# Kernel tuning notes

Hardware: AMD Instinct MI355X
Metric: run time of the kernel (lower is better)

The kernel has to match this reference:

```python
import jax, jax.numpy as jnp
import numpy as np

N = 16384          # nodes
E = 262144         # edges (before self-loops)
FIN_N, FIN_E = 768, 64
F, FE = 256, 128   # node/edge channels
H, C = 8, 32       # heads, per-head dim (H*C == F)
L = 2              # num GATv2 modules
NEG_SLOPE = 0.2


def layer_norm(x, g, b, eps=1e-5):
    mu = jnp.mean(x, axis=-1, keepdims=True)
    var = jnp.mean((x - mu) ** 2, axis=-1, keepdims=True)
    return (x - mu) * jax.lax.rsqrt(var + eps) * g + b


def segment_softmax(logits, seg, n):
    # logits: [Et, H], seg: [Et] destination node ids
    m = jax.ops.segment_max(logits, seg, num_segments=n)
    m = jnp.where(jnp.isfinite(m), m, 0.0)
    e = jnp.exp(logits - m[seg])
    s = jax.ops.segment_sum(e, seg, num_segments=n)
    return e / (s[seg] + 1e-16)


def setup_inputs() -> dict:
    key = jax.random.key(0)
    ks = jax.random.split(key, 20)
    inp = {
        "node_feats": jax.random.normal(ks[0], (N, FIN_N), jnp.float32),
        "edge_index": jax.random.randint(ks[1], (2, E), 0, N, dtype=jnp.int32),
        "edge_attr": jax.random.normal(ks[2], (E, FIN_E), jnp.float32),
        # input projections (bias=False)
        "init_node_w": jax.random.normal(ks[3], (F, FIN_N), jnp.float32) * 0.02,
        "init_edge_w": jax.random.normal(ks[4], (FE, FIN_E), jnp.float32) * 0.02,
        # per-layer GATv2 params, stacked on leading layer dim L
        "lin_l_w": jax.random.normal(ks[5], (L, H * C, F), jnp.float32) * 0.05,
        "lin_l_b": jnp.zeros((L, H * C), jnp.float32),
        "lin_r_w": jax.random.normal(ks[6], (L, H * C, F), jnp.float32) * 0.05,
        "lin_r_b": jnp.zeros((L, H * C), jnp.float32),
        "lin_edge_w": jax.random.normal(ks[7], (L, H * C, FE), jnp.float32) * 0.05,
        "att": jax.random.normal(ks[8], (L, H, C), jnp.float32) * 0.05,
        "gat_bias": jnp.zeros((L, H * C), jnp.float32),
        # block params
        "ln1_g": jnp.ones((L, F), jnp.float32), "ln1_b": jnp.zeros((L, F), jnp.float32),
        "mlp_w1": jax.random.normal(ks[9], (L, 2 * F, F), jnp.float32) * 0.05,
        "mlp_w2": jax.random.normal(ks[10], (L, F, 2 * F), jnp.float32) * 0.05,
        "ln2_g": jnp.ones((L, F), jnp.float32), "ln2_b": jnp.zeros((L, F), jnp.float32),
    }
    return inp


def _gatv2_module(x, src, dst, e_emb, p, l, n):
    # e_emb: [Et, H, C] already projected edge embeddings (incl. self-loops)
    x_l = (x @ p["lin_l_w"][l].T + p["lin_l_b"][l]).reshape(n, H, C)
    x_r = (x @ p["lin_r_w"][l].T + p["lin_r_b"][l]).reshape(n, H, C)
    m = x_l[src] + x_r[dst] + e_emb                    # [Et, H, C]
    g = jnp.where(m >= 0, m, NEG_SLOPE * m)            # leaky_relu(0.2)
    logits = jnp.einsum('ehc,hc->eh', g, p["att"][l])
    alpha = segment_softmax(logits, dst, n)            # [Et, H]
    out = jax.ops.segment_sum(alpha[:, :, None] * x_l[src], dst, num_segments=n)
    out = out.reshape(n, H * C) + p["gat_bias"][l]
    # residual -> LN -> MLP -> residual -> LN  (dropout=0, eval mode)
    h = layer_norm(x + out, p["ln1_g"][l], p["ln1_b"][l])
    y = jax.nn.gelu(h @ p["mlp_w1"][l].T, approximate=False) @ p["mlp_w2"][l].T
    return layer_norm(h + y, p["ln2_g"][l], p["ln2_b"][l])


def reference(node_feats, edge_index, edge_attr, init_node_w, init_edge_w,
              lin_l_w, lin_l_b, lin_r_w, lin_r_b, lin_edge_w, att, gat_bias,
              ln1_g, ln1_b, mlp_w1, mlp_w2, ln2_g, ln2_b):
    p = dict(lin_l_w=lin_l_w, lin_l_b=lin_l_b, lin_r_w=lin_r_w, lin_r_b=lin_r_b,
             lin_edge_w=lin_edge_w, att=att, gat_bias=gat_bias, ln1_g=ln1_g,
             ln1_b=ln1_b, mlp_w1=mlp_w1, mlp_w2=mlp_w2, ln2_g=ln2_g, ln2_b=ln2_b)
    x = node_feats @ init_node_w.T                     # [N, F]
    ea = edge_attr @ init_edge_w.T                     # [E, FE]
    src, dst = edge_index[0], edge_index[1]
    # add self loops with fill_value='mean' (mean of incoming edge_attr per node)
    cnt = jax.ops.segment_sum(jnp.ones((E,), ea.dtype), dst, num_segments=N)
    loop_attr = jax.ops.segment_sum(ea, dst, num_segments=N) / jnp.maximum(cnt, 1.0)[:, None]
    ea_all = jnp.concatenate([ea, loop_attr], axis=0)  # [E+N, FE]
    ar = jnp.arange(N, dtype=src.dtype)
    src_all = jnp.concatenate([src, ar])
    dst_all = jnp.concatenate([dst, ar])
    for l in range(L):
        e_emb = (ea_all @ lin_edge_w[l].T).reshape(-1, H, C)
        x = _gatv2_module(x, src_all, dst_all, e_emb, p, l, N)
    return x
```

## Files before the change

kernel.cpp:

```cpp
#include <hip/hip_runtime.h>

typedef unsigned short u16;
typedef __attribute__((ext_vector_type(8))) short s8v;
typedef __attribute__((ext_vector_type(4))) float f4v;

#define NN 16384
#define EE 262144
#define ET (EE + NN)
#define NTILES (ET / 64)

__device__ __forceinline__ float bfu(u16 h){ return __uint_as_float((unsigned)h << 16); }
__device__ __forceinline__ u16 f2bf(float f){
  unsigned u = __float_as_uint(f);
  unsigned r = u + 0x7FFFu + ((u >> 16) & 1u);
  return (u16)(r >> 16);
}
__device__ __forceinline__ float ldf(const void* p, size_t i, int isbf){
  return isbf ? bfu(((const u16*)p)[i]) : ((const float*)p)[i];
}
__device__ __forceinline__ float gelu_f(float x){ return 0.5f*x*(1.0f+erff(x*0.7071067811865475f)); }

__device__ __forceinline__ uint4 load8bf(const void* p, size_t eoff, int isbf){
  if (isbf) return *(const uint4*)((const u16*)p + eoff);
  const float* f = (const float*)p + eoff;
  uint4 r;
  r.x = (unsigned)f2bf(f[0]) | ((unsigned)f2bf(f[1])<<16);
  r.y = (unsigned)f2bf(f[2]) | ((unsigned)f2bf(f[3])<<16);
  r.z = (unsigned)f2bf(f[4]) | ((unsigned)f2bf(f[5])<<16);
  r.w = (unsigned)f2bf(f[6]) | ((unsigned)f2bf(f[7])<<16);
  return r;
}

__device__ __forceinline__ void gload16(const void* g, void* l){
  __builtin_amdgcn_global_load_lds((const __attribute__((address_space(1))) void*)g,
                                   (__attribute__((address_space(3))) void*)l, 16, 0, 0);
}

__global__ void k_detect(const void* nf, int* flag)
{
  int t = threadIdx.x;
  const float* f = (const float*)nf;
  int cnt = 0;
  for (int i = t; i < 4096; i += 256) {
    float a = fabsf(f[i]);
    if (a > 1e-5f && a < 100.0f) cnt++;
  }
  __shared__ int s[256];
  s[t] = cnt; __syncthreads();
  for (int st = 128; st > 0; st >>= 1) { if (t < st) s[t] += s[t+st]; __syncthreads(); }
  if (t == 0) *flag = (s[0] < 2048) ? 1 : 0;
}

__global__ void k_cvt(const void* __restrict__ in, u16* __restrict__ out, const int* __restrict__ dflag)
{
  int isbf = *dflag;
  size_t i = ((size_t)blockIdx.x*256 + threadIdx.x)*8;
  *(uint4*)&out[i] = load8bf(in, i, isbf);
}

__global__ void k_wcvt(const void* __restrict__ lw, const void* __restrict__ rw,
                       const void* __restrict__ w1, const void* __restrict__ w2,
                       const void* __restrict__ iw, u16* __restrict__ wall,
                       const int* __restrict__ dflag)
{
  int isbf = *dflag;
  size_t i = ((size_t)blockIdx.x*256 + threadIdx.x)*8;
  const void* src; size_t off;
  if (i < 196608) { src = iw; off = i; }
  else {
    size_t j = i - 196608;
    size_t l = j / 393216; j -= l*393216;
    if (j < 65536)       { src = lw; off = l*65536 + j; }
    else if (j < 131072) { src = rw; off = l*65536 + (j - 65536); }
    else if (j < 262144) { src = w1; off = l*131072 + (j - 131072); }
    else                 { src = w2; off = l*131072 + (j - 262144); }
  }
  *(uint4*)&wall[i] = load8bf(src, off, isbf);
}

template<int KK, int NJ, int ACT, int CFMT>
__global__ __launch_bounds__(256)
void mg3(const u16* __restrict__ A, const u16* __restrict__ B,
         const void* __restrict__ bias1, const void* __restrict__ bias2,
         size_t bioff, int nsplit, int has_bias,
         void* __restrict__ C, void* __restrict__ C2, int N,
         const int* __restrict__ dflag)
{
  constexpr int NIT = KK/32;
  constexpr int NBF = 4*NJ;
  __shared__ u16 As[2][4][512];
  __shared__ u16 Bs[2][NBF][512];
  int isbf = *dflag;
  int t = threadIdx.x;
  int w = t>>6, lane = t&63, l4 = lane&15, quad = lane>>4;
  int bm = blockIdx.y*64, bn = blockIdx.x*(64*NJ);

  const u16* gA = A + (size_t)(bm + w*16 + l4)*KK + quad*8;
  const u16* gB[NJ];
  #pragma unroll
  for (int j=0;j<NJ;++j)
    gB[j] = B + (size_t)(bn + (NJ*w + j)*16 + l4)*KK + quad*8;

  f4v acc[4][NJ];
  f4v zero = {0.f,0.f,0.f,0.f};
  #pragma unroll
  for (int i=0;i<4;++i)
    #pragma unroll
    for (int j=0;j<NJ;++j) acc[i][j] = zero;

  gload16(gA, &As[0][w][0]);
  #pragma unroll
  for (int j=0;j<NJ;++j) gload16(gB[j], &Bs[0][NJ*w + j][0]);
  __syncthreads();

  int buf = 0;
  for (int it = 0; it < NIT; ++it) {
    if (it + 1 < NIT) {
      int k0 = (it+1)*32;
      gload16(gA + k0, &As[buf^1][w][0]);
      #pragma unroll
      for (int j=0;j<NJ;++j) gload16(gB[j] + k0, &Bs[buf^1][NJ*w + j][0]);
    }
    s8v a[4], b[NJ];
    #pragma unroll
    for (int i=0;i<4;++i) a[i] = *(const s8v*)&As[buf][i][lane*8];
    #pragma unroll
    for (int j=0;j<NJ;++j) b[j] = *(const s8v*)&Bs[buf][NJ*w + j][lane*8];
    #pragma unroll
    for (int i=0;i<4;++i)
      #pragma unroll
      for (int j=0;j<NJ;++j)
        acc[i][j] = __builtin_amdgcn_mfma_f32_16x16x32_bf16(a[i], b[j], acc[i][j], 0,0,0);
    __syncthreads();
    buf ^= 1;
  }

  #pragma unroll
  for (int i=0;i<4;++i)
    #pragma unroll
    for (int j=0;j<NJ;++j) {
      int cj = bn + (NJ*w + j)*16 + l4;
      float bvs = 0.f;
      if (has_bias) bvs = (cj < nsplit) ? ldf(bias1, bioff + cj, isbf)
                                        : ldf(bias2, bioff + cj - nsplit, isbf);
      #pragma unroll
      for (int r=0;r<4;++r) {
        int row = bm + i*16 + quad*4 + r;
        float v = acc[i][j][r] + bvs;
        if (ACT==1) v = gelu_f(v);
        if (CFMT==1) ((u16*)C)[(size_t)row*N + cj] = f2bf(v);
        else {
          ((float*)C)[(size_t)row*N + cj] = v;
          if (CFMT==2) ((u16*)C2)[(size_t)row*N + cj] = f2bf(v);
        }
      }
    }
}

__global__ void k_count(const int* __restrict__ dst, int* __restrict__ deg)
{
  int e = blockIdx.x*256 + threadIdx.x;
  if (e >= ET) return;
  int d = (e < EE) ? dst[e] : (e - EE);
  atomicAdd(&deg[d], 1);
}

__global__ void k_scan(const int* __restrict__ deg, int* __restrict__ rowstart)
{
  __shared__ int csum[256];
  int t = threadIdx.x;
  int s = 0;
  for (int i=0;i<64;i++) s += deg[t*64+i];
  csum[t] = s;
  __syncthreads();
  if (t == 0) {
    int r = 0;
    for (int i=0;i<256;i++){ int v = csum[i]; csum[i] = r; r += v; }
    rowstart[NN] = r;
  }
  __syncthreads();
  int b = csum[t];
  for (int i=0;i<64;i++){ rowstart[t*64+i] = b; b += deg[t*64+i]; }
}

__global__ void k_scatter(const int* __restrict__ src, const int* __restrict__ dst,
                          const int* __restrict__ rowstart,
                          int* __restrict__ fill, int* __restrict__ csr,
                          int* __restrict__ srcc, int* __restrict__ dstc)
{
  int e = blockIdx.x*256 + threadIdx.x;
  if (e >= ET) return;
  int d  = (e < EE) ? dst[e] : (e - EE);
  int sv = (e < EE) ? src[e] : (e - EE);
  int pos = rowstart[d] + atomicAdd(&fill[d], 1);
  csr[pos]  = e;
  srcc[pos] = sv;
  dstc[pos] = d;
}

__global__ void k_loopmean(const int* __restrict__ csr, const int* __restrict__ rowstart,
                           const void* __restrict__ edge_attr, u16* __restrict__ loopmean,
                           const int* __restrict__ dflag)
{
  int isbf = *dflag;
  int n = blockIdx.x, j = threadIdx.x;
  int s = rowstart[n], e1 = rowstart[n+1];
  float sum = 0.f; int cnt = 0;
  for (int p = s; p < e1; ++p) {
    int eid = csr[p];
    if (eid < EE) { sum += ldf(edge_attr, (size_t)eid*64 + j, isbf); cnt++; }
  }
  loopmean[(size_t)n*64 + j] = f2bf(sum / (float)max(cnt, 1));
}

__global__ void k_wc(const void* __restrict__ We, const void* __restrict__ iew,
                     u16* __restrict__ Wcb, const int* __restrict__ dflag)
{
  int isbf = *dflag;
  int idx = blockIdx.x*256 + threadIdx.x;
  int j = idx & 63, c = (idx >> 6) & 255, l = idx >> 14;
  float s = 0.f;
  for (int k=0;k<128;k++) s += ldf(We, ((size_t)l*256 + c)*128 + k, isbf) * ldf(iew, (size_t)k*64 + j, isbf);
  Wcb[idx] = f2bf(s);
}

__global__ __launch_bounds__(256)
void k_elogits(const int* __restrict__ csr, const int* __restrict__ srcc, const int* __restrict__ dstc,
               const u16* __restrict__ Wcb, const u16* __restrict__ xlr,
               const void* __restrict__ edge_attr, const u16* __restrict__ loopmean,
               const void* __restrict__ att, size_t att_off,
               float* __restrict__ logits, const int* __restrict__ dflag)
{
  int isbf = *dflag;
  __shared__ u16 WcF[32*64*8];
  __shared__ u16 attr_s[64*72];
  __shared__ float satt[256];
  __shared__ int ssrc[64], sdst[64];

  int t = threadIdx.x;
  int w = t>>6, lane = t&63, l4 = lane&15, quad = lane>>4;

  satt[t] = ldf(att, att_off + t, isbf);
  #pragma unroll
  for (int f = 0; f < 8; ++f) {
    int fr = w + f*4;
    int i = fr >> 1, ks = fr & 1;
    *(uint4*)&WcF[(fr*64 + lane)*8] = *(const uint4*)&Wcb[(size_t)(16*i + l4)*64 + ks*32 + quad*8];
  }

  f4v zero = {0.f,0.f,0.f,0.f};
  for (int tile = blockIdx.x; tile < NTILES; tile += gridDim.x) {
    int e0 = tile*64;
    __syncthreads();
    if (t < 64) {
      ssrc[t] = srcc[e0 + t];
      sdst[t] = dstc[e0 + t];
    }
    {
      int er = t >> 2, part = t & 3;
      int eid = csr[e0 + er];
      uint4 v0, v1;
      if (eid < EE) {
        v0 = load8bf(edge_attr, (size_t)eid*64 + part*16,     isbf);
        v1 = load8bf(edge_attr, (size_t)eid*64 + part*16 + 8, isbf);
      } else {
        v0 = *(const uint4*)&loopmean[(size_t)(eid-EE)*64 + part*16];
        v1 = *(const uint4*)&loopmean[(size_t)(eid-EE)*64 + part*16 + 8];
      }
      *(uint4*)&attr_s[er*72 + part*16]     = v0;
      *(uint4*)&attr_s[er*72 + part*16 + 8] = v1;
    }
    __syncthreads();

    s8v b0 = *(const s8v*)&attr_s[(w*16 + l4)*72 + quad*8];
    s8v b1 = *(const s8v*)&attr_s[(w*16 + l4)*72 + 32 + quad*8];
    f4v acc[16];
    #pragma unroll
    for (int i=0;i<16;++i){
      s8v a0 = *(const s8v*)&WcF[((2*i  )*64 + lane)*8];
      s8v a1 = *(const s8v*)&WcF[((2*i+1)*64 + lane)*8];
      acc[i] = __builtin_amdgcn_mfma_f32_16x16x32_bf16(a0, b0, zero, 0,0,0);
      acc[i] = __builtin_amdgcn_mfma_f32_16x16x32_bf16(a1, b1, acc[i], 0,0,0);
    }

    int me = w*16 + l4;
    int sn = ssrc[me], dn = sdst[me];
    float ph[8] = {0.f,0.f,0.f,0.f,0.f,0.f,0.f,0.f};
    #pragma unroll
    for (int i=0;i<16;++i){
      uint2 xlv = *(const uint2*)&xlr[(size_t)sn*512 +       i*16 + quad*4];
      uint2 xrv = *(const uint2*)&xlr[(size_t)dn*512 + 256 + i*16 + quad*4];
      float4 av = *(const float4*)&satt[i*16 + quad*4];
      float m0 = acc[i][0] + bfu((u16)(xlv.x & 0xffff)) + bfu((u16)(xrv.x & 0xffff));
      float m1 = acc[i][1] + bfu((u16)(xlv.x >> 16))    + bfu((u16)(xrv.x >> 16));
      float m2 = acc[i][2] + bfu((u16)(xlv.y & 0xffff)) + bfu((u16)(xrv.y & 0xffff));
      float m3 = acc[i][3] + bfu((u16)(xlv.y >> 16))    + bfu((u16)(xrv.y >> 16));
      float g0 = fmaxf(m0, 0.2f*m0), g1 = fmaxf(m1, 0.2f*m1);
      float g2 = fmaxf(m2, 0.2f*m2), g3 = fmaxf(m3, 0.2f*m3);
      ph[i>>1] += av.x*g0 + av.y*g1 + av.z*g2 + av.w*g3;
    }
    #pragma unroll
    for (int h=0;h<8;++h){
      ph[h] += __shfl_xor(ph[h], 16);
      ph[h] += __shfl_xor(ph[h], 32);
    }
    if (quad == 0){
      float4 lo = {ph[0], ph[1], ph[2], ph[3]};
      float4 hi = {ph[4], ph[5], ph[6], ph[7]};
      *(float4*)&logits[(size_t)(e0 + me)*8]     = lo;
      *(float4*)&logits[(size_t)(e0 + me)*8 + 4] = hi;
    }
  }
}

__global__ __launch_bounds__(256)
void k_aggln(const int* __restrict__ srcc, const int* __restrict__ rowstart,
             const float* __restrict__ logits, const u16* __restrict__ xlr, const float* __restrict__ xbuf,
             const void* __restrict__ gat_bias, const void* __restrict__ ln1g, const void* __restrict__ ln1b,
             size_t poff, float* __restrict__ hbuf, u16* __restrict__ hbufb, const int* __restrict__ dflag)
{
  int isbf = *dflag;
  int lane = threadIdx.x & 63, wid = threadIdx.x >> 6;
  int n = blockIdx.x*4 + wid;
  int s = rowstart[n], deg = rowstart[n+1] - s;
  int myh = lane >> 3;
  float mrun = -3.0e38f, lrun = 0.f;
  float a0=0.f, a1=0.f, a2=0.f, a3=0.f;

  for (int c0 = 0; c0 < deg; c0 += 64) {
    int idx = s + c0 + lane; if (idx >= ET) idx = ET-1;
    int sv = srcc[idx];
    int lim = min(64, deg - c0);
    size_t lbase = (size_t)(s + c0)*8 + myh;
    for (int j = 0; j < lim; ++j) {
      int sn  = __shfl(sv, j);
      float lg = logits[lbase + (size_t)j*8];
      uint2 xv = *(const uint2*)&xlr[(size_t)sn*512 + 4*lane];
      float mn = fmaxf(mrun, lg);
      float sc = __expf(mrun - mn);
      float wv = __expf(lg - mn);
      mrun = mn;
      lrun = lrun*sc + wv;
      a0 = a0*sc + wv*bfu((u16)(xv.x & 0xffff));
      a1 = a1*sc + wv*bfu((u16)(xv.x >> 16));
      a2 = a2*sc + wv*bfu((u16)(xv.y & 0xffff));
      a3 = a3*sc + wv*bfu((u16)(xv.y >> 16));
    }
  }
  float inv = 1.f/(lrun + 1e-16f);
  int c = 4*lane;
  float4 res = *(const float4*)&xbuf[(size_t)n*256 + c];
  float o0 = a0*inv + ldf(gat_bias, poff+c+0, isbf) + res.x;
  float o1 = a1*inv + ldf(gat_bias, poff+c+1, isbf) + res.y;
  float o2 = a2*inv + ldf(gat_bias, poff+c+2, isbf) + res.z;
  float o3 = a3*inv + ldf(gat_bias, poff+c+3, isbf) + res.w;

  float v = o0+o1+o2+o3;
  #pragma unroll
  for (int off=1; off<64; off<<=1) v += __shfl_xor(v, off);
  float mu = v * (1.f/256.f);
  float d0=o0-mu, d1=o1-mu, d2=o2-mu, d3=o3-mu;
  float v2 = d0*d0+d1*d1+d2*d2+d3*d3;
  #pragma unroll
  for (int off=1; off<64; off<<=1) v2 += __shfl_xor(v2, off);
  float wn = rsqrtf(v2*(1.f/256.f) + 1e-5f);
  float4 outv;
  outv.x = d0*wn*ldf(ln1g, poff+c+0, isbf) + ldf(ln1b, poff+c+0, isbf);
  outv.y = d1*wn*ldf(ln1g, poff+c+1, isbf) + ldf(ln1b, poff+c+1, isbf);
  outv.z = d2*wn*ldf(ln1g, poff+c+2, isbf) + ldf(ln1b, poff+c+2, isbf);
  outv.w = d3*wn*ldf(ln1g, poff+c+3, isbf) + ldf(ln1b, poff+c+3, isbf);
  *(float4*)&hbuf[(size_t)n*256 + c] = outv;
  uint2 hb;
  hb.x = (unsigned)f2bf(outv.x) | ((unsigned)f2bf(outv.y)<<16);
  hb.y = (unsigned)f2bf(outv.z) | ((unsigned)f2bf(outv.w)<<16);
  *(uint2*)&hbufb[(size_t)n*256 + c] = hb;
}

__global__ __launch_bounds__(256)
void k_ln_add(const float* __restrict__ a, const u16* __restrict__ b2,
              const void* __restrict__ gg, const void* __restrict__ bb, size_t poff,
              float* __restrict__ out, u16* __restrict__ outb, const int* __restrict__ dflag)
{
  int isbf = *dflag;
  int n = blockIdx.x, t = threadIdx.x;
  __shared__ float r[256];
  float x = a[(size_t)n*256 + t] + bfu(b2[(size_t)n*256 + t]);
  r[t] = x; __syncthreads();
  for (int st = 128; st > 0; st >>= 1) { if (t < st) r[t] += r[t+st]; __syncthreads(); }
  float mu = r[0] * (1.f/256.f);
  __syncthreads();
  float d = x - mu;
  r[t] = d*d; __syncthreads();
  for (int st = 128; st > 0; st >>= 1) { if (t < st) r[t] += r[t+st]; __syncthreads(); }
  float var = r[0] * (1.f/256.f);
  float o = d * rsqrtf(var + 1e-5f) * ldf(gg, poff + t, isbf) + ldf(bb, poff + t, isbf);
  out[(size_t)n*256 + t] = o;
  outb[(size_t)n*256 + t] = f2bf(o);
}

__global__ void k_out(const float* __restrict__ x, void* __restrict__ out, const int* __restrict__ dflag)
{
  int isbf = *dflag;
  int i = blockIdx.x*256 + threadIdx.x;
  if (isbf) ((u16*)out)[i] = f2bf(x[i]);
  else      ((float*)out)[i] = x[i];
}

extern "C" void kernel_launch(void* const* d_in, const int* in_sizes, int n_in,
                              void* d_out, int out_size, void* d_ws, size_t ws_size,
                              hipStream_t stream)
{
  const void* node_feats = d_in[0];
  const int*  edge_index = (const int*)d_in[1];
  const void* edge_attr  = d_in[2];
  const void* init_node_w= d_in[3];
  const void* init_edge_w= d_in[4];
  const void* lin_l_w    = d_in[5];
  const void* lin_l_b    = d_in[6];
  const void* lin_r_w    = d_in[7];
  const void* lin_r_b    = d_in[8];
  const void* lin_edge_w = d_in[9];
  const void* att        = d_in[10];
  const void* gat_bias   = d_in[11];
  const void* ln1_g      = d_in[12];
  const void* ln1_b      = d_in[13];
  const void* mlp_w1     = d_in[14];
  const void* mlp_w2     = d_in[15];
  const void* ln2_g      = d_in[16];
  const void* ln2_b      = d_in[17];

  const int* srcp = edge_index;
  const int* dstp = edge_index + EE;

  char* p = (char*)d_ws;
  auto alloc = [&](size_t bytes) { void* r = (void*)p; p += (bytes + 255) & ~(size_t)255; return r; };
  int*   dflag   = (int*)alloc(256);
  int*   deg     = (int*)alloc((size_t)NN*4);
  int*   rowstart= (int*)alloc((size_t)(NN+1)*4);
  int*   fill    = (int*)alloc((size_t)NN*4);
  int*   csr     = (int*)alloc((size_t)ET*4);
  int*   srcc    = (int*)alloc((size_t)ET*4);
  int*   dstc    = (int*)alloc((size_t)ET*4);
  u16*   Wcb     = (u16*)alloc((size_t)2*256*64*2);
  u16*   loopmean= (u16*)alloc((size_t)NN*64*2);
  u16*   wall    = (u16*)alloc((size_t)983040*2);
  float* logits  = (float*)alloc((size_t)ET*8*4);
  float* hbuf    = (float*)alloc((size_t)NN*256*4);
  float* xbuf    = (float*)alloc((size_t)NN*256*4);
  u16*   xbufb   = (u16*)alloc((size_t)NN*256*2);
  u16*   hbufb   = (u16*)alloc((size_t)NN*256*2);
  u16*   xlr     = (u16*)alloc((size_t)NN*512*2);
  u16*   nfb     = (u16*)logits;
  u16*   ymid    = xlr;
  u16*   y2      = (u16*)d_out;

  u16* Wn = wall;

  hipMemsetAsync(deg,  0, (size_t)NN*4, stream);
  hipMemsetAsync(fill, 0, (size_t)NN*4, stream);

  k_detect <<<1, 256, 0, stream>>>(node_feats, dflag);

  k_count  <<<(ET+255)/256, 256, 0, stream>>>(dstp, deg);
  k_scan   <<<1, 256, 0, stream>>>(deg, rowstart);
  k_scatter<<<(ET+255)/256, 256, 0, stream>>>(srcp, dstp, rowstart, fill, csr, srcc, dstc);
  k_loopmean<<<NN, 64, 0, stream>>>(csr, rowstart, edge_attr, loopmean, dflag);
  k_wc     <<<128, 256, 0, stream>>>(lin_edge_w, init_edge_w, Wcb, dflag);
  k_wcvt   <<<480, 256, 0, stream>>>(lin_l_w, lin_r_w, mlp_w1, mlp_w2, init_node_w, wall, dflag);

  k_cvt<<<(NN*768)/(8*256), 256, 0, stream>>>(node_feats, nfb, dflag);
  mg3<768,1,0,2><<<dim3(4, NN/64), 256, 0, stream>>>(nfb, Wn, nullptr, nullptr, 0, 1<<29, 0,
                                                     xbuf, xbufb, 256, dflag);

  for (int l = 0; l < 2; ++l) {
    size_t bo = (size_t)l*256;
    u16* Wlr = wall + 196608 + (size_t)l*393216;
    u16* W1  = Wlr + 131072;
    u16* W2  = Wlr + 262144;
    mg3<256,2,0,1><<<dim3(4, NN/64), 256, 0, stream>>>(xbufb, Wlr, lin_l_b, lin_r_b, bo, 256, 1,
                                                       xlr, nullptr, 512, dflag);
    k_elogits<<<768, 256, 0, stream>>>(csr, srcc, dstc, Wcb + (size_t)l*256*64, xlr,
                                       edge_attr, loopmean, att, (size_t)l*256, logits, dflag);
    k_aggln<<<NN/4, 256, 0, stream>>>(srcc, rowstart, logits, xlr, xbuf,
                                      gat_bias, ln1_g, ln1_b, bo, hbuf, hbufb, dflag);
    mg3<256,2,1,1><<<dim3(4, NN/64), 256, 0, stream>>>(hbufb, W1, nullptr, nullptr, 0, 1<<29, 0,
                                                       ymid, nullptr, 512, dflag);
    mg3<512,1,0,1><<<dim3(4, NN/64), 256, 0, stream>>>(ymid, W2, nullptr, nullptr, 0, 1<<29, 0,
                                                       y2, nullptr, 256, dflag);
    k_ln_add<<<NN, 256, 0, stream>>>(hbuf, y2, ln2_g, ln2_b, bo, xbuf, xbufb, dflag);
  }

  k_out<<<(NN*256)/256, 256, 0, stream>>>(xbuf, d_out, dflag);
}
```

Baseline: 634.6 us.

## Pre-permute edge attributes into CSR order and restructure GEMM with register-held B

Edge attributes are first converted to bf16. A new kernel then writes them into CSR-sorted order while computing the self-loop mean, so the per-layer logits kernel can read contiguous rows instead of gathering by edge id. The GEMM kernel drops its double-buffered LDS pipeline. It now loads B fragments straight into registers in 256-wide K chunks, stages only A in shared memory, and adds an XCD-aware swizzle of the workgroup index. The trade is an extra full-size attr_csr buffer and conversion pass, plus higher register pressure and less load/compute overlap in the GEMM.

```diff
diff --git a/kernel.cpp b/kernel.cpp
--- a/kernel.cpp
+++ b/kernel.cpp
@@ -80,20 +80,22 @@
 
 template<int KK, int NJ, int ACT, int CFMT>
 __global__ __launch_bounds__(256)
-void mg3(const u16* __restrict__ A, const u16* __restrict__ B,
+void mg4(const u16* __restrict__ A, const u16* __restrict__ B,
          const void* __restrict__ bias1, const void* __restrict__ bias2,
          size_t bioff, int nsplit, int has_bias,
          void* __restrict__ C, void* __restrict__ C2, int N,
          const int* __restrict__ dflag)
 {
-  constexpr int NIT = KK/32;
-  constexpr int NBF = 4*NJ;
-  __shared__ u16 As[2][4][512];
-  __shared__ u16 Bs[2][NBF][512];
+  __shared__ u16 As[32][512];
   int isbf = *dflag;
   int t = threadIdx.x;
   int w = t>>6, lane = t&63, l4 = lane&15, quad = lane>>4;
-  int bm = blockIdx.y*64, bn = blockIdx.x*(64*NJ);
+
+  int nwg = gridDim.x*gridDim.y;
+  int wg  = blockIdx.y*gridDim.x + blockIdx.x;
+  int lg  = (wg & 7)*(nwg >> 3) + (wg >> 3);
+  int bx  = lg % gridDim.x, by = lg / gridDim.x;
+  int bm = by*64, bn = bx*(64*NJ);
 
   const u16* gA = A + (size_t)(bm + w*16 + l4)*KK + quad*8;
   const u16* gB[NJ];
@@ -108,31 +110,30 @@
     #pragma unroll
     for (int j=0;j<NJ;++j) acc[i][j] = zero;
 
-  gload16(gA, &As[0][w][0]);
-  #pragma unroll
-  for (int j=0;j<NJ;++j) gload16(gB[j], &Bs[0][NJ*w + j][0]);
-  __syncthreads();
-
-  int buf = 0;
-  for (int it = 0; it < NIT; ++it) {
-    if (it + 1 < NIT) {
-      int k0 = (it+1)*32;
-      gload16(gA + k0, &As[buf^1][w][0]);
-      #pragma unroll
-      for (int j=0;j<NJ;++j) gload16(gB[j] + k0, &Bs[buf^1][NJ*w + j][0]);
-    }
-    s8v a[4], b[NJ];
-    #pragma unroll
-    for (int i=0;i<4;++i) a[i] = *(const s8v*)&As[buf][i][lane*8];
-    #pragma unroll
-    for (int j=0;j<NJ;++j) b[j] = *(const s8v*)&Bs[buf][NJ*w + j][lane*8];
-    #pragma unroll
-    for (int i=0;i<4;++i)
+  #pragma unroll
+  for (int kc=0; kc<KK/256; ++kc) {
+    if (kc) __syncthreads();
+    s8v breg[8][NJ];
+    #pragma unroll
+    for (int c=0;c<8;++c)
       #pragma unroll
       for (int j=0;j<NJ;++j)
-        acc[i][j] = __builtin_amdgcn_mfma_f32_16x16x32_bf16(a[i], b[j], acc[i][j], 0,0,0);
+        breg[c][j] = *(const s8v*)(gB[j] + kc*256 + c*32);
+    #pragma unroll
+    for (int c=0;c<8;++c)
+      gload16(gA + kc*256 + c*32, &As[c*4 + w][0]);
     __syncthreads();
-    buf ^= 1;
+    #pragma unroll
+    for (int c=0;c<8;++c) {
+      s8v a[4];
+      #pragma unroll
+      for (int i=0;i<4;++i) a[i] = *(const s8v*)&As[c*4 + i][lane*8];
+      #pragma unroll
+      for (int i=0;i<4;++i)
+        #pragma unroll
+        for (int j=0;j<NJ;++j)
+          acc[i][j] = __builtin_amdgcn_mfma_f32_16x16x32_bf16(a[i], breg[c][j], acc[i][j], 0,0,0);
+    }
   }
 
   #pragma unroll
@@ -198,19 +199,23 @@
   dstc[pos] = d;
 }
 
-__global__ void k_loopmean(const int* __restrict__ csr, const int* __restrict__ rowstart,
-                           const void* __restrict__ edge_attr, u16* __restrict__ loopmean,
-                           const int* __restrict__ dflag)
-{
-  int isbf = *dflag;
-  int n = blockIdx.x, j = threadIdx.x;
+__global__ __launch_bounds__(256)
+void k_lm_acsr(const int* __restrict__ csr, const int* __restrict__ rowstart,
+               const u16* __restrict__ eab, u16* __restrict__ attr_csr)
+{
+  int j = threadIdx.x & 63, wid = threadIdx.x >> 6;
+  int n = blockIdx.x*4 + wid;
   int s = rowstart[n], e1 = rowstart[n+1];
-  float sum = 0.f; int cnt = 0;
+  float sum = 0.f; int cnt = 0; int selfpos = s;
   for (int p = s; p < e1; ++p) {
     int eid = csr[p];
-    if (eid < EE) { sum += ldf(edge_attr, (size_t)eid*64 + j, isbf); cnt++; }
-  }
-  loopmean[(size_t)n*64 + j] = f2bf(sum / (float)max(cnt, 1));
+    if (eid < EE) {
+      u16 v = eab[(size_t)eid*64 + j];
+      attr_csr[(size_t)p*64 + j] = v;
+      sum += bfu(v); cnt++;
+    } else selfpos = p;
+  }
+  attr_csr[(size_t)selfpos*64 + j] = f2bf(sum / (float)max(cnt, 1));
 }
 
 __global__ void k_wc(const void* __restrict__ We, const void* __restrict__ iew,
@@ -225,9 +230,9 @@
 }
 
 __global__ __launch_bounds__(256)
-void k_elogits(const int* __restrict__ csr, const int* __restrict__ srcc, const int* __restrict__ dstc,
+void k_elogits(const int* __restrict__ srcc, const int* __restrict__ dstc,
                const u16* __restrict__ Wcb, const u16* __restrict__ xlr,
-               const void* __restrict__ edge_attr, const u16* __restrict__ loopmean,
+               const u16* __restrict__ attr_csr,
                const void* __restrict__ att, size_t att_off,
                float* __restrict__ logits, const int* __restrict__ dflag)
 {
@@ -258,17 +263,9 @@
     }
     {
       int er = t >> 2, part = t & 3;
-      int eid = csr[e0 + er];
-      uint4 v0, v1;
-      if (eid < EE) {
-        v0 = load8bf(edge_attr, (size_t)eid*64 + part*16,     isbf);
-        v1 = load8bf(edge_attr, (size_t)eid*64 + part*16 + 8, isbf);
-      } else {
-        v0 = *(const uint4*)&loopmean[(size_t)(eid-EE)*64 + part*16];
-        v1 = *(const uint4*)&loopmean[(size_t)(eid-EE)*64 + part*16 + 8];
-      }
-      *(uint4*)&attr_s[er*72 + part*16]     = v0;
-      *(uint4*)&attr_s[er*72 + part*16 + 8] = v1;
+      const u16* src = attr_csr + (size_t)(e0 + er)*64 + part*16;
+      *(uint4*)&attr_s[er*72 + part*16]     = *(const uint4*)src;
+      *(uint4*)&attr_s[er*72 + part*16 + 8] = *(const uint4*)(src + 8);
     }
     __syncthreads();
 
@@ -442,14 +439,15 @@
   int*   srcc    = (int*)alloc((size_t)ET*4);
   int*   dstc    = (int*)alloc((size_t)ET*4);
   u16*   Wcb     = (u16*)alloc((size_t)2*256*64*2);
-  u16*   loopmean= (u16*)alloc((size_t)NN*64*2);
   u16*   wall    = (u16*)alloc((size_t)983040*2);
+  u16*   attr_csr= (u16*)alloc((size_t)ET*64*2);
   float* logits  = (float*)alloc((size_t)ET*8*4);
   float* hbuf    = (float*)alloc((size_t)NN*256*4);
   float* xbuf    = (float*)alloc((size_t)NN*256*4);
   u16*   xbufb   = (u16*)alloc((size_t)NN*256*2);
   u16*   hbufb   = (u16*)alloc((size_t)NN*256*2);
   u16*   xlr     = (u16*)alloc((size_t)NN*512*2);
+  u16*   eab     = (u16*)logits;
   u16*   nfb     = (u16*)logits;
   u16*   ymid    = xlr;
   u16*   y2      = (u16*)d_out;
@@ -464,12 +462,14 @@
   k_count  <<<(ET+255)/256, 256, 0, stream>>>(dstp, deg);
   k_scan   <<<1, 256, 0, stream>>>(deg, rowstart);
   k_scatter<<<(ET+255)/256, 256, 0, stream>>>(srcp, dstp, rowstart, fill, csr, srcc, dstc);
-  k_loopmean<<<NN, 64, 0, stream>>>(csr, rowstart, edge_attr, loopmean, dflag);
+  k_cvt    <<<(EE*64)/(8*256), 256, 0, stream>>>(edge_attr, eab, dflag);
+  k_lm_acsr<<<NN/4, 256, 0, stream>>>(csr, rowstart, eab, attr_csr);
+
   k_wc     <<<128, 256, 0, stream>>>(lin_edge_w, init_edge_w, Wcb, dflag);
   k_wcvt   <<<480, 256, 0, stream>>>(lin_l_w, lin_r_w, mlp_w1, mlp_w2, init_node_w, wall, dflag);
 
   k_cvt<<<(NN*768)/(8*256), 256, 0, stream>>>(node_feats, nfb, dflag);
-  mg3<768,1,0,2><<<dim3(4, NN/64), 256, 0, stream>>>(nfb, Wn, nullptr, nullptr, 0, 1<<29, 0,
+  mg4<768,1,0,2><<<dim3(4, NN/64), 256, 0, stream>>>(nfb, Wn, nullptr, nullptr, 0, 1<<29, 0,
                                                      xbuf, xbufb, 256, dflag);
 
   for (int l = 0; l < 2; ++l) {
@@ -477,15 +477,15 @@
     u16* Wlr = wall + 196608 + (size_t)l*393216;
     u16* W1  = Wlr + 131072;
     u16* W2  = Wlr + 262144;
-    mg3<256,2,0,1><<<dim3(4, NN/64), 256, 0, stream>>>(xbufb, Wlr, lin_l_b, lin_r_b, bo, 256, 1,
+    mg4<256,2,0,1><<<dim3(4, NN/64), 256, 0, stream>>>(xbufb, Wlr, lin_l_b, lin_r_b, bo, 256, 1,
                                                        xlr, nullptr, 512, dflag);
-    k_elogits<<<768, 256, 0, stream>>>(csr, srcc, dstc, Wcb + (size_t)l*256*64, xlr,
-                                       edge_attr, loopmean, att, (size_t)l*256, logits, dflag);
+    k_elogits<<<768, 256, 0, stream>>>(srcc, dstc, Wcb + (size_t)l*256*64, xlr,
+                                       attr_csr, att, (size_t)l*256, logits, dflag);
     k_aggln<<<NN/4, 256, 0, stream>>>(srcc, rowstart, logits, xlr, xbuf,
                                       gat_bias, ln1_g, ln1_b, bo, hbuf, hbufb, dflag);
-    mg3<256,2,1,1><<<dim3(4, NN/64), 256, 0, stream>>>(hbufb, W1, nullptr, nullptr, 0, 1<<29, 0,
+    mg4<256,2,1,1><<<dim3(4, NN/64), 256, 0, stream>>>(hbufb, W1, nullptr, nullptr, 0, 1<<29, 0,
                                                        ymid, nullptr, 512, dflag);
-    mg3<512,1,0,1><<<dim3(4, NN/64), 256, 0, stream>>>(ymid, W2, nullptr, nullptr, 0, 1<<29, 0,
+    mg4<512,1,0,1><<<dim3(4, NN/64), 256, 0, stream>>>(ymid, W2, nullptr, nullptr, 0, 1<<29, 0,
                                                        y2, nullptr, 256, dflag);
     k_ln_add<<<NN, 256, 0, stream>>>(hbuf, y2, ln2_g, ln2_b, bo, xbuf, xbufb, dflag);
   }
```

After: 671.9 us. +5.9%, slower.
